# Optimization experiments

Hardware: AMD Instinct MI355X
Metric: run time of the kernel (lower is better)

## Reference

```python
import jax, jax.numpy as jnp
import numpy as np

RANK = 192      # wbits=4 -> rank 192 in prepare_grouped_lora
QMAX = 15.0     # 2**4 - 1 for 4-bit asymmetric quantization
EPS = 1e-8

def _fake_quant_weight(w):
    # Per-output-channel asymmetric min-max fake quantization (4-bit).
    wmin = jnp.minimum(w.min(axis=1, keepdims=True), 0.0)
    wmax = jnp.maximum(w.max(axis=1, keepdims=True), 0.0)
    scale = jnp.maximum((wmax - wmin) / QMAX, EPS)
    zero = jnp.round(-wmin / scale)
    q = jnp.clip(jnp.round(w / scale) + zero, 0.0, QMAX)
    return (q - zero) * scale

def setup_inputs() -> dict:
    key = jax.random.key(0)
    k1, k2, k3, k4, k5 = jax.random.split(key, 5)
    B, S, IN, OUT = 4, 2048, 4096, 11008
    x = jax.random.normal(k1, (B, S, IN), dtype=jnp.float32)
    weight = jax.random.normal(k2, (OUT, IN), dtype=jnp.float32) * 0.02
    Bd = jax.random.normal(k3, (OUT, RANK), dtype=jnp.float32) * 0.01
    Bu = jax.random.normal(k4, (RANK, IN), dtype=jnp.float32) * 0.01
    bias = jax.random.normal(k5, (OUT,), dtype=jnp.float32) * 0.01
    return {"x": x, "weight": weight, "Bd": Bd, "Bu": Bu, "bias": bias}

def reference(x, weight, Bd, Bu, bias):
    # LoRA delta: Bd[:, :rank] @ Bu[:rank, :]  (rank=192 for 4-bit)
    delta = jnp.einsum('or,ri->oi', Bd[:, :RANK], Bu[:RANK, :])
    w = _fake_quant_weight(weight + delta)          # [out, in]
    out = jnp.einsum('bsi,oi->bso', x, w) + bias    # F.linear
    return out
```

## Files before the change

### kernel.cpp

```cpp
#include <hip/hip_runtime.h>
#include <stdint.h>

#define M_ROWS 8192
#define N_OUT  11008
#define K_IN   4096
#define RANK   192

typedef __attribute__((ext_vector_type(8))) short bf16x8;
typedef __attribute__((ext_vector_type(4))) float f32x4;

#define GLDS16(g, l) __builtin_amdgcn_global_load_lds( \
    (const __attribute__((address_space(1))) unsigned int*)(g), \
    (__attribute__((address_space(3))) unsigned int*)(l), 16, 0, 0)

static __device__ __forceinline__ unsigned short f2bf(float f) {
    union { float f; unsigned int u; } a; a.f = f;
    unsigned int u = a.u;
    u += 0x7fffu + ((u >> 16) & 1u);
    return (unsigned short)(u >> 16);
}

__global__ __launch_bounds__(256) void k_delta_minmax(
    const float* __restrict__ Wg, const float* __restrict__ Bd,
    const float* __restrict__ Bu, float* __restrict__ wq,
    float* __restrict__ pmin, float* __restrict__ pmax)
{
    __shared__ float bdT[RANK][68];
    __shared__ float buS[8][256];
    const int t  = threadIdx.x;
    const int tx = t & 31, ty = t >> 5;
    const int row0 = blockIdx.x * 64;
    const int col0 = blockIdx.y * 256;

    for (int i = t; i < 64 * RANK; i += 256) {
        int r = i / RANK, k = i - r * RANK;
        bdT[k][r] = Bd[(size_t)(row0 + r) * RANK + k];
    }

    float acc[8][8];
#pragma unroll
    for (int a = 0; a < 8; ++a)
#pragma unroll
        for (int b = 0; b < 8; ++b) acc[a][b] = 0.0f;

    for (int kc = 0; kc < RANK / 8; ++kc) {
        __syncthreads();
#pragma unroll
        for (int j = 0; j < 8; ++j)
            buS[j][t] = Bu[(size_t)(kc * 8 + j) * K_IN + col0 + t];
        __syncthreads();
#pragma unroll
        for (int k = 0; k < 8; ++k) {
            float bd[8], bu[8];
#pragma unroll
            for (int rr = 0; rr < 8; ++rr) bd[rr] = bdT[kc * 8 + k][ty * 8 + rr];
#pragma unroll
            for (int cc = 0; cc < 8; ++cc) bu[cc] = buS[k][tx + 32 * cc];
#pragma unroll
            for (int rr = 0; rr < 8; ++rr)
#pragma unroll
                for (int cc = 0; cc < 8; ++cc)
                    acc[rr][cc] = fmaf(bd[rr], bu[cc], acc[rr][cc]);
        }
    }

    float rmin[8], rmax[8];
#pragma unroll
    for (int rr = 0; rr < 8; ++rr) { rmin[rr] = 3.0e38f; rmax[rr] = -3.0e38f; }
#pragma unroll
    for (int rr = 0; rr < 8; ++rr) {
        size_t gr = (size_t)(row0 + ty * 8 + rr);
#pragma unroll
        for (int cc = 0; cc < 8; ++cc) {
            size_t gc = (size_t)(col0 + tx + 32 * cc);
            float w = Wg[gr * K_IN + gc] + acc[rr][cc];
            wq[gr * K_IN + gc] = w;
            rmin[rr] = fminf(rmin[rr], w);
            rmax[rr] = fmaxf(rmax[rr], w);
        }
    }
#pragma unroll
    for (int off = 16; off >= 1; off >>= 1) {
#pragma unroll
        for (int rr = 0; rr < 8; ++rr) {
            rmin[rr] = fminf(rmin[rr], __shfl_xor(rmin[rr], off, 64));
            rmax[rr] = fmaxf(rmax[rr], __shfl_xor(rmax[rr], off, 64));
        }
    }
    if (tx == 0) {
#pragma unroll
        for (int rr = 0; rr < 8; ++rr) {
            int gr = row0 + ty * 8 + rr;
            pmin[(size_t)gr * 16 + blockIdx.y] = rmin[rr];
            pmax[(size_t)gr * 16 + blockIdx.y] = rmax[rr];
        }
    }
}

__global__ __launch_bounds__(256) void k_scale_zero(
    const float* __restrict__ pmin, const float* __restrict__ pmax,
    float* __restrict__ scale, float* __restrict__ zero)
{
    int r = blockIdx.x * 256 + threadIdx.x;
    if (r >= N_OUT) return;
    float mn = 0.0f, mx = 0.0f;
#pragma unroll
    for (int i = 0; i < 16; ++i) {
        mn = fminf(mn, pmin[(size_t)r * 16 + i]);
        mx = fmaxf(mx, pmax[(size_t)r * 16 + i]);
    }
    float s = fmaxf((mx - mn) / 15.0f, 1e-8f);
    scale[r] = s;
    zero[r] = rintf(-mn / s);
}

__global__ __launch_bounds__(256) void k_quant_cast(
    const float* __restrict__ wq, const float* __restrict__ scale,
    const float* __restrict__ zero, unsigned short* __restrict__ wb)
{
    size_t i = ((size_t)blockIdx.x * 256 + threadIdx.x) * 4;
    int r = (int)(i >> 12);
    float s = scale[r], z = zero[r];
    float4 v = *(const float4*)(wq + i);
    float in[4] = {v.x, v.y, v.z, v.w};
    unsigned short h[4];
#pragma unroll
    for (int j = 0; j < 4; ++j) {
        float q = rintf(in[j] / s) + z;
        q = fminf(fmaxf(q, 0.0f), 15.0f);
        h[j] = f2bf((q - z) * s);
    }
    unsigned int lo = (unsigned int)h[0] | ((unsigned int)h[1] << 16);
    unsigned int hi = (unsigned int)h[2] | ((unsigned int)h[3] << 16);
    *(unsigned long long*)(wb + i) = ((unsigned long long)hi << 32) | lo;
}

__global__ __launch_bounds__(256) void k_cast_x(
    const float* __restrict__ x, unsigned short* __restrict__ xb)
{
    size_t i = ((size_t)blockIdx.x * 256 + threadIdx.x) * 4;
    float4 v = *(const float4*)(x + i);
    unsigned int lo = (unsigned int)f2bf(v.x) | ((unsigned int)f2bf(v.y) << 16);
    unsigned int hi = (unsigned int)f2bf(v.z) | ((unsigned int)f2bf(v.w) << 16);
    *(unsigned long long*)(xb + i) = ((unsigned long long)hi << 32) | lo;
}

__global__ __launch_bounds__(256) void k_gemm(
    const unsigned short* __restrict__ A,
    const unsigned short* __restrict__ W,
    const float* __restrict__ bias,
    float* __restrict__ C)
{
    __shared__ alignas(16) char lds_a[128 * 64];
    __shared__ alignas(16) char lds_b[128 * 64];
    const int t    = threadIdx.x;
    const int lane = t & 63;
    const int wave = t >> 6;
    const int wr = wave >> 1, wc = wave & 1;
    const int bm0 = blockIdx.x * 128;
    const int bn0 = blockIdx.y * 128;

    const int sr = t >> 2;
    const int sk = (t & 3) * 8;
    const unsigned short* gA = A + (size_t)(bm0 + sr) * K_IN + sk;
    const unsigned short* gW = W + (size_t)(bn0 + sr) * K_IN + sk;
    char* sA = lds_a + wave * 1024;
    char* sB = lds_b + wave * 1024;

    f32x4 acc[4][4];
    const f32x4 zf = {0.f, 0.f, 0.f, 0.f};
#pragma unroll
    for (int i = 0; i < 4; ++i)
#pragma unroll
        for (int j = 0; j < 4; ++j) acc[i][j] = zf;

    const int lrow = lane & 15, lq = lane >> 4;
    const int aoff = (wr * 64 + lrow) * 64 + lq * 16;
    const int boff = (wc * 64 + lrow) * 64 + lq * 16;

    for (int kt = 0; kt < K_IN / 32; ++kt) {
        GLDS16(gA,                      sA);
        GLDS16(gA + (size_t)64 * K_IN,  sA + 4096);
        GLDS16(gW,                      sB);
        GLDS16(gW + (size_t)64 * K_IN,  sB + 4096);
        gA += 32; gW += 32;
        __syncthreads();

        bf16x8 af[4], bfr[4];
#pragma unroll
        for (int mi = 0; mi < 4; ++mi)
            af[mi] = *(const bf16x8*)(lds_a + aoff + mi * 1024);
#pragma unroll
        for (int ni = 0; ni < 4; ++ni)
            bfr[ni] = *(const bf16x8*)(lds_b + boff + ni * 1024);
#pragma unroll
        for (int mi = 0; mi < 4; ++mi)
#pragma unroll
            for (int ni = 0; ni < 4; ++ni)
                acc[mi][ni] = __builtin_amdgcn_mfma_f32_16x16x32_bf16(
                    af[mi], bfr[ni], acc[mi][ni], 0, 0, 0);
        __syncthreads();
    }

#pragma unroll
    for (int mi = 0; mi < 4; ++mi) {
        const int row = bm0 + wr * 64 + mi * 16 + lq * 4;
#pragma unroll
        for (int ni = 0; ni < 4; ++ni) {
            const int col = bn0 + wc * 64 + ni * 16 + lrow;
            const float bb = bias[col];
#pragma unroll
            for (int r = 0; r < 4; ++r)
                C[(size_t)(row + r) * N_OUT + col] = acc[mi][ni][r] + bb;
        }
    }
}

extern "C" void kernel_launch(void* const* d_in, const int* in_sizes, int n_in,
                              void* d_out, int out_size, void* d_ws, size_t ws_size,
                              hipStream_t stream)
{
    const float* x      = (const float*)d_in[0];
    const float* weight = (const float*)d_in[1];
    const float* Bd     = (const float*)d_in[2];
    const float* Bu     = (const float*)d_in[3];
    const float* bias   = (const float*)d_in[4];
    float* out = (float*)d_out;

    char* ws = (char*)d_ws;
    float*          wq    = (float*)(ws);
    float*          pmin  = (float*)(ws + 180355072);
    float*          pmax  = (float*)(ws + 181059584);
    float*          scale = (float*)(ws + 181764096);
    float*          zero  = (float*)(ws + 181808128);
    unsigned short* wb    = (unsigned short*)(ws + 181852160);
    unsigned short* xb    = (unsigned short*)(ws + 272029696);

    k_delta_minmax<<<dim3(N_OUT / 64, K_IN / 256), 256, 0, stream>>>(
        weight, Bd, Bu, wq, pmin, pmax);
    k_scale_zero<<<(N_OUT + 255) / 256, 256, 0, stream>>>(pmin, pmax, scale, zero);
    k_quant_cast<<<(N_OUT * (K_IN / 4)) / 256, 256, 0, stream>>>(wq, scale, zero, wb);
    k_cast_x<<<(M_ROWS * (K_IN / 4)) / 256, 256, 0, stream>>>(x, xb);
    k_gemm<<<dim3(M_ROWS / 128, N_OUT / 128), 256, 0, stream>>>(xb, wb, bias, out);
}
```

Before: 1.884 ms.

## Rewrite bf16 GEMM as 256x256 tile, 8-wave, double-buffered LDS pipeline

Replaces the 128x128, 4-wave, K=32 single-buffer GEMM with a 256x256 tile computed by 8 waves, K=64 per step, and two LDS buffers of 64KB each in dynamic shared memory. Global-to-LDS loads for upcoming tiles are interleaved with MFMA quarters, separated by explicit barriers and vmcnt waits, and the MFMA sections raise wave priority. It also XOR-swizzles LDS columns to avoid bank conflicts and remaps block indices for better L2 locality. The aim is to hide memory latency and raise arithmetic intensity. The cost is 128KB of LDS per block and tight hand-tuned wait counts that could break correctness if miscounted.

Result: faster. 1.708 ms (-9.4%).

```diff
diff --git a/kernel.cpp b/kernel.cpp
--- a/kernel.cpp
+++ b/kernel.cpp
@@ -145,73 +145,129 @@
     *(unsigned long long*)(xb + i) = ((unsigned long long)hi << 32) | lo;
 }
 
-__global__ __launch_bounds__(256) void k_gemm(
+#define NT (K_IN / 64)
+
+__global__ __launch_bounds__(512, 2) void k_gemm(
     const unsigned short* __restrict__ A,
     const unsigned short* __restrict__ W,
     const float* __restrict__ bias,
     float* __restrict__ C)
 {
-    __shared__ alignas(16) char lds_a[128 * 64];
-    __shared__ alignas(16) char lds_b[128 * 64];
-    const int t    = threadIdx.x;
-    const int lane = t & 63;
-    const int wave = t >> 6;
-    const int wr = wave >> 1, wc = wave & 1;
-    const int bm0 = blockIdx.x * 128;
-    const int bn0 = blockIdx.y * 128;
-
-    const int sr = t >> 2;
-    const int sk = (t & 3) * 8;
-    const unsigned short* gA = A + (size_t)(bm0 + sr) * K_IN + sk;
-    const unsigned short* gW = W + (size_t)(bn0 + sr) * K_IN + sk;
-    char* sA = lds_a + wave * 1024;
-    char* sB = lds_b + wave * 1024;
-
-    f32x4 acc[4][4];
-    const f32x4 zf = {0.f, 0.f, 0.f, 0.f};
-#pragma unroll
-    for (int i = 0; i < 4; ++i)
-#pragma unroll
-        for (int j = 0; j < 4; ++j) acc[i][j] = zf;
+    extern __shared__ char lds[];
+
+    const int tid  = threadIdx.x;
+    const int lane = tid & 63;
+    const int w    = tid >> 6;
+    const int wr   = w >> 2;
+    const int wn   = w & 3;
+
+    const int orig = blockIdx.y * gridDim.x + blockIdx.x;
+    const int swz  = (orig & 7) * 172 + (orig >> 3);
+    const int bm0  = (swz & 31) << 8;
+    const int bn0  = (swz >> 5) << 8;
 
     const int lrow = lane & 15, lq = lane >> 4;
-    const int aoff = (wr * 64 + lrow) * 64 + lq * 16;
-    const int boff = (wc * 64 + lrow) * 64 + lq * 16;
-
-    for (int kt = 0; kt < K_IN / 32; ++kt) {
-        GLDS16(gA,                      sA);
-        GLDS16(gA + (size_t)64 * K_IN,  sA + 4096);
-        GLDS16(gW,                      sB);
-        GLDS16(gW + (size_t)64 * K_IN,  sB + 4096);
-        gA += 32; gW += 32;
-        __syncthreads();
-
-        bf16x8 af[4], bfr[4];
-#pragma unroll
-        for (int mi = 0; mi < 4; ++mi)
-            af[mi] = *(const bf16x8*)(lds_a + aoff + mi * 1024);
-#pragma unroll
-        for (int ni = 0; ni < 4; ++ni)
-            bfr[ni] = *(const bf16x8*)(lds_b + boff + ni * 1024);
-#pragma unroll
-        for (int mi = 0; mi < 4; ++mi)
-#pragma unroll
-            for (int ni = 0; ni < 4; ++ni)
-                acc[mi][ni] = __builtin_amdgcn_mfma_f32_16x16x32_bf16(
-                    af[mi], bfr[ni], acc[mi][ni], 0, 0, 0);
-        __syncthreads();
-    }
-
+    const int colA = (lq * 16) ^ (((lrow >> 3) & 1) << 5);
+
+    const int srow = w * 16 + (lane >> 2);
+    const int scol = ((lane & 3) * 8) ^ (((lane >> 5) & 1) * 16);
+
+    const unsigned short* pa = A + (size_t)(bm0 + srow) * K_IN + scol;
+    const unsigned short* pw = W + (size_t)(bn0 + srow) * K_IN + scol;
+    char* ldsw = lds + w * 1024;
+
+    char* abase = lds + (wr * 64 + lrow) * 64 + colA;
+    char* bbase = lds + 32768 + (wn * 32 + lrow) * 64 + colA;
+
+#define STAGE_A(D, KT, H) { \
+    const unsigned short* s_ = pa + (size_t)((H) * 128) * K_IN + (KT) * 64; \
+    char* l_ = ldsw + (D) * 65536 + (H) * 16384; \
+    GLDS16(s_,      l_); \
+    GLDS16(s_ + 32, l_ + 8192); }
+#define STAGE_B(D, KT, H) { \
+    const unsigned short* s_ = pw + (size_t)((H) * 128) * K_IN + (KT) * 64; \
+    char* l_ = ldsw + (D) * 65536 + 32768 + (H) * 16384; \
+    GLDS16(s_,      l_); \
+    GLDS16(s_ + 32, l_ + 8192); }
+
+#define READ_A(D, MH) { \
+    _Pragma("unroll") for (int mi = 0; mi < 4; ++mi) { \
+        af[mi][0] = *(const bf16x8*)(abase + (D) * 65536 + (MH) * 16384 + mi * 1024); \
+        af[mi][1] = *(const bf16x8*)(abase + (D) * 65536 + (MH) * 16384 + 8192 + mi * 1024); } }
+#define READ_B(D, NH, B_) { \
+    _Pragma("unroll") for (int ni = 0; ni < 2; ++ni) { \
+        B_[ni][0] = *(const bf16x8*)(bbase + (D) * 65536 + (NH) * 16384 + ni * 1024); \
+        B_[ni][1] = *(const bf16x8*)(bbase + (D) * 65536 + (NH) * 16384 + 8192 + ni * 1024); } }
+
+#define MFMA_Q(MH, NH, B_) { \
+    __builtin_amdgcn_s_setprio(1); \
+    _Pragma("unroll") for (int mi = 0; mi < 4; ++mi) \
+    _Pragma("unroll") for (int ni = 0; ni < 2; ++ni) { \
+        acc[MH][NH][mi][ni] = __builtin_amdgcn_mfma_f32_16x16x32_bf16( \
+            af[mi][0], B_[ni][0], acc[MH][NH][mi][ni], 0, 0, 0); \
+        acc[MH][NH][mi][ni] = __builtin_amdgcn_mfma_f32_16x16x32_bf16( \
+            af[mi][1], B_[ni][1], acc[MH][NH][mi][ni], 0, 0, 0); } \
+    __builtin_amdgcn_s_setprio(0); }
+
+    f32x4 acc[2][2][4][2] = {};
+    bf16x8 af[4][2], b0[2][2], b1[2][2];
+
+    STAGE_A(0, 0, 0); STAGE_A(0, 0, 1); STAGE_B(0, 0, 0); STAGE_B(0, 0, 1);
+    STAGE_A(1, 1, 0); STAGE_B(1, 1, 1); STAGE_A(1, 1, 1);
+    asm volatile("s_waitcnt vmcnt(6)" ::: "memory");
+    __builtin_amdgcn_s_barrier();
+
+#define TILE_BODY(T, D, DN) { \
+     \
+    READ_A(D, 0); READ_B(D, 0, b0); \
+    if ((T) + 1 < NT) STAGE_B(DN, (T) + 1, 0); \
+    __builtin_amdgcn_s_barrier(); \
+    MFMA_Q(0, 0, b0); \
+    __builtin_amdgcn_s_barrier(); \
+     \
+    READ_B(D, 1, b1); \
+    if ((T) + 2 < NT) STAGE_A(D, (T) + 2, 0); \
+    __builtin_amdgcn_s_barrier(); \
+    MFMA_Q(0, 1, b1); \
+    __builtin_amdgcn_s_barrier(); \
+     \
+    READ_A(D, 1); \
+    if ((T) + 2 < NT) STAGE_B(D, (T) + 2, 1); \
+    __builtin_amdgcn_s_barrier(); \
+    MFMA_Q(1, 1, b1); \
+    __builtin_amdgcn_s_barrier(); \
+     \
+    if ((T) + 2 < NT) { \
+        STAGE_A(D, (T) + 2, 1); \
+        asm volatile("s_waitcnt vmcnt(6)" ::: "memory"); \
+    } else { \
+        asm volatile("s_waitcnt vmcnt(0)" ::: "memory"); \
+    } \
+    __builtin_amdgcn_s_barrier(); \
+    MFMA_Q(1, 0, b0); \
+    __builtin_amdgcn_s_barrier(); }
+
+#pragma unroll 1
+    for (int tt = 0; tt < NT; tt += 2) {
+        TILE_BODY(tt,     0, 1);
+        TILE_BODY(tt + 1, 1, 0);
+    }
+
+#pragma unroll
+    for (int mh = 0; mh < 2; ++mh)
 #pragma unroll
     for (int mi = 0; mi < 4; ++mi) {
-        const int row = bm0 + wr * 64 + mi * 16 + lq * 4;
-#pragma unroll
-        for (int ni = 0; ni < 4; ++ni) {
-            const int col = bn0 + wc * 64 + ni * 16 + lrow;
+        const int row = bm0 + mh * 128 + wr * 64 + mi * 16 + lq * 4;
+#pragma unroll
+        for (int nh = 0; nh < 2; ++nh)
+#pragma unroll
+        for (int ni = 0; ni < 2; ++ni) {
+            const int col = bn0 + nh * 128 + wn * 32 + ni * 16 + lrow;
             const float bb = bias[col];
+            const f32x4 v = acc[mh][nh][mi][ni];
 #pragma unroll
             for (int r = 0; r < 4; ++r)
-                C[(size_t)(row + r) * N_OUT + col] = acc[mi][ni][r] + bb;
+                C[(size_t)(row + r) * N_OUT + col] = v[r] + bb;
         }
     }
 }
@@ -236,10 +292,17 @@
     unsigned short* wb    = (unsigned short*)(ws + 181852160);
     unsigned short* xb    = (unsigned short*)(ws + 272029696);
 
+    static bool attr_set = false;
+    if (!attr_set) {
+        hipFuncSetAttribute((const void*)k_gemm,
+                            hipFuncAttributeMaxDynamicSharedMemorySize, 131072);
+        attr_set = true;
+    }
+
     k_delta_minmax<<<dim3(N_OUT / 64, K_IN / 256), 256, 0, stream>>>(
         weight, Bd, Bu, wq, pmin, pmax);
     k_scale_zero<<<(N_OUT + 255) / 256, 256, 0, stream>>>(pmin, pmax, scale, zero);
     k_quant_cast<<<(N_OUT * (K_IN / 4)) / 256, 256, 0, stream>>>(wq, scale, zero, wb);
     k_cast_x<<<(M_ROWS * (K_IN / 4)) / 256, 256, 0, stream>>>(x, xb);
-    k_gemm<<<dim3(M_ROWS / 128, N_OUT / 128), 256, 0, stream>>>(xb, wb, bias, out);
-}
+    k_gemm<<<dim3(M_ROWS / 256, N_OUT / 256), 512, 131072, stream>>>(xb, wb, bias, out);
+}
```
